# Performance work log

Measured on AMD Instinct MI355X. Metric: run time of the kernel, lower is better.

Reference implementation:

```python
import jax, jax.numpy as jnp
import numpy as np

D_MODEL = 1280
NUM_EXPERTS = 20
HEAD_DIM = D_MODEL // NUM_EXPERTS  # 64
SCALE = HEAD_DIM ** -0.5


def setup_inputs() -> dict:
    key = jax.random.key(0)
    ks = jax.random.split(key, 8)
    B, S = 4, 1024
    s_in = 1.0 / np.sqrt(D_MODEL)
    x = jax.random.normal(ks[0], (B, S, D_MODEL), dtype=jnp.float32)
    # per-expert QKV projections stacked: [E, d_model, 3*head_dim]
    wqkv = jax.random.uniform(ks[1], (NUM_EXPERTS, D_MODEL, 3 * HEAD_DIM), jnp.float32, -s_in, s_in)
    bqkv = jax.random.uniform(ks[2], (NUM_EXPERTS, 3 * HEAD_DIM), jnp.float32, -s_in, s_in)
    router_w = jax.random.uniform(ks[3], (D_MODEL, NUM_EXPERTS), jnp.float32, -s_in, s_in)
    router_b = jax.random.uniform(ks[4], (NUM_EXPERTS,), jnp.float32, -s_in, s_in)
    out_w = jax.random.uniform(ks[5], (D_MODEL, D_MODEL), jnp.float32, -s_in, s_in)
    out_b = jax.random.uniform(ks[6], (D_MODEL,), jnp.float32, -s_in, s_in)
    return {"x": x, "wqkv": wqkv, "bqkv": bqkv, "router_w": router_w,
            "router_b": router_b, "out_w": out_w, "out_b": out_b}


def reference(x, wqkv, bqkv, router_w, router_b, out_w, out_b):
    # x: [B, S, D]
    B, S, D = x.shape
    E, H = NUM_EXPERTS, HEAD_DIM
    # router softmax gates (dropout = identity in eval)
    gates = jax.nn.softmax(x @ router_w + router_b, axis=-1)  # [B, S, E]
    # per-expert QKV: [E, B, S, 3H]
    qkv = jnp.einsum('bsd,edh->ebsh', x, wqkv) + bqkv[:, None, None, :]
    q, k, v = jnp.split(qkv, 3, axis=-1)  # each [E, B, S, H]
    scores = jnp.einsum('ebqh,ebkh->ebqk', q, k) * SCALE  # [E, B, S, S]
    attn = jax.nn.softmax(scores, axis=-1)
    eo = jnp.einsum('ebqk,ebkh->ebqh', attn, v)  # [E, B, S, H]
    # gate multiply and scatter into disjoint feature slices == concat over experts
    eo = eo * jnp.transpose(gates, (2, 0, 1))[..., None]  # [E, B, S, H]
    combined = jnp.transpose(eo, (1, 2, 0, 3)).reshape(B, S, E * H)  # [B, S, D]
    return combined @ out_w + out_b
```

## Files before the change

### kernel.cpp

```cpp
#include <hip/hip_runtime.h>
#include <hip/hip_bf16.h>

#define D_MODEL 1280
#define NUM_EXPERTS 20
#define HEAD_DIM 64
#define SEQ 1024
#define BATCH 4
#define BS_TOK 4096
#define QKV_N 192
#define QKV_W 3840

typedef __attribute__((ext_vector_type(8))) short short8;
typedef __attribute__((ext_vector_type(4))) float f32x4;
typedef __attribute__((ext_vector_type(16))) float f32x16;
typedef __hip_bfloat16 bf16;

static __device__ __forceinline__ void gload_lds16(const void* g, void* l) {
  __builtin_amdgcn_global_load_lds((const __attribute__((address_space(1))) void*)g,
                                   (__attribute__((address_space(3))) void*)l, 16, 0, 0);
}

__global__ __launch_bounds__(256) void k_rwT(const float* __restrict__ in,
                                             float* __restrict__ out) {
  int i = blockIdx.x * 256 + threadIdx.x;
  if (i < D_MODEL * NUM_EXPERTS) {
    int d = i / NUM_EXPERTS, e = i % NUM_EXPERTS;
    out[e * D_MODEL + d] = in[i];
  }
}

__global__ __launch_bounds__(256) void k_gates(const float* __restrict__ x,
    const float* __restrict__ rwT, const float* __restrict__ rb,
    float* __restrict__ gates, bf16* __restrict__ xb)
{
  __shared__ float xs[4][D_MODEL];
  __shared__ float logits[4][NUM_EXPERTS];
  const int r0 = blockIdx.x * 4;
  for (int i = threadIdx.x; i < 4 * (D_MODEL / 2); i += 256) {
    int r = i / (D_MODEL / 2), d2 = (i % (D_MODEL / 2)) * 2;
    float2 v = *(const float2*)(x + (size_t)(r0 + r) * D_MODEL + d2);
    xs[r][d2] = v.x; xs[r][d2 + 1] = v.y;
    __hip_bfloat162 h;
    h.x = __float2bfloat16(v.x); h.y = __float2bfloat16(v.y);
    *(__hip_bfloat162*)(xb + (size_t)(r0 + r) * D_MODEL + d2) = h;
  }
  __syncthreads();
  const int wid = threadIdx.x >> 6, lane = threadIdx.x & 63;
  for (int e = 0; e < NUM_EXPERTS; ++e) {
    float s = 0.f;
    #pragma unroll
    for (int j = 0; j < D_MODEL / 64; ++j) {
      int d = lane + 64 * j;
      s += xs[wid][d] * rwT[e * D_MODEL + d];
    }
    #pragma unroll
    for (int m = 32; m >= 1; m >>= 1) s += __shfl_xor(s, m);
    if (lane == 0) logits[wid][e] = s + rb[e];
  }
  __syncthreads();
  if (lane < 32) {
    float v = (lane < NUM_EXPERTS) ? logits[wid][lane] : -1e30f;
    float mx = v;
    #pragma unroll
    for (int m = 16; m >= 1; m >>= 1) mx = fmaxf(mx, __shfl_xor(mx, m, 32));
    float p = (lane < NUM_EXPERTS) ? __expf(v - mx) : 0.f;
    float sum = p;
    #pragma unroll
    for (int m = 16; m >= 1; m >>= 1) sum += __shfl_xor(sum, m, 32);
    if (lane < NUM_EXPERTS)
      gates[(size_t)(r0 + wid) * NUM_EXPERTS + lane] = p / sum;
  }
}

__global__ __launch_bounds__(256) void k_transpose(const float* __restrict__ in,
    bf16* __restrict__ out, int R, int C)
{
  __shared__ float tile[32][33];
  const size_t bo = (size_t)blockIdx.z * R * C;
  const int c0 = blockIdx.x * 32, r0 = blockIdx.y * 32;
  const int tx = threadIdx.x, ty = threadIdx.y;
  #pragma unroll
  for (int i = 0; i < 4; ++i)
    tile[ty + 8*i][tx] = in[bo + (size_t)(r0 + ty + 8*i) * C + (c0 + tx)];
  __syncthreads();
  #pragma unroll
  for (int i = 0; i < 4; ++i)
    out[bo + (size_t)(c0 + ty + 8*i) * R + (r0 + tx)] =
        __float2bfloat16(tile[tx][ty + 8*i]);
}

__global__ __launch_bounds__(512, 2) void k_gemm256(
    const bf16* __restrict__ A, const bf16* __restrict__ BT,
    const float* __restrict__ bias, bf16* __restrict__ C,
    int M, int N, int K)
{
  __shared__ __align__(16) bf16 lds[4][2][256 * 32];
  const int bid = blockIdx.x;
  const int xcd = bid & 7, c = bid >> 3;
  const int m0 = (xcd * 2 + (c & 1)) * 256;
  const int n0 = (c >> 1) * 256;
  const int tid = threadIdx.x, wid = tid >> 6, lane = tid & 63;
  const int wr = wid >> 2, wcn = wid & 3;
  const int fr = lane & 15, fg = lane >> 4;
  const int nt = K / 32;

  auto STAGE = [&](int t, int buf) {
    const bf16* Ag = A + (size_t)m0 * K + t * 32;
    const bf16* Bg = BT + (size_t)n0 * K + t * 32;
    #pragma unroll
    for (int i = 0; i < 2; ++i) {
      int idx = i * 512 + tid;
      int row = idx >> 2, sc = idx & 3;
      int g = sc ^ (row & 3);
      gload_lds16(Ag + (size_t)row * K + g * 8, &lds[buf][0][idx * 8]);
    }
    #pragma unroll
    for (int i = 0; i < 2; ++i) {
      int idx = i * 512 + tid;
      int row = idx >> 2, sc = idx & 3;
      int g = sc ^ (row & 3);
      gload_lds16(Bg + (size_t)row * K + g * 8, &lds[buf][1][idx * 8]);
    }
  };

  f32x4 acc[8][4] = {};
  auto COMPUTE = [&](int buf) {
    const bf16* As_ = &lds[buf][0][0];
    const bf16* Bs_ = &lds[buf][1][0];
    short8 af[8], bfv[4];
    #pragma unroll
    for (int mi = 0; mi < 8; ++mi) {
      int row = wr * 128 + mi * 16 + fr;
      int slot = fg ^ (row & 3);
      af[mi] = *(const short8*)(As_ + row * 32 + slot * 8);
    }
    #pragma unroll
    for (int ni = 0; ni < 4; ++ni) {
      int row = wcn * 64 + ni * 16 + fr;
      int slot = fg ^ (row & 3);
      bfv[ni] = *(const short8*)(Bs_ + row * 32 + slot * 8);
    }
    __builtin_amdgcn_s_setprio(1);
    #pragma unroll
    for (int mi = 0; mi < 8; ++mi) {
      #pragma unroll
      for (int ni = 0; ni < 4; ++ni)
        acc[mi][ni] = __builtin_amdgcn_mfma_f32_16x16x32_bf16(
            af[mi], bfv[ni], acc[mi][ni], 0, 0, 0);
    }
    __builtin_amdgcn_s_setprio(0);
  };

  STAGE(0, 0); STAGE(1, 1); STAGE(2, 2);
  asm volatile("s_waitcnt vmcnt(8)" ::: "memory");
  __builtin_amdgcn_s_barrier();
  __builtin_amdgcn_sched_barrier(0);
  int buf = 0;
  for (int t = 0; t < nt - 3; ++t) {
    int nb = buf + 3; nb = (nb >= 4) ? nb - 4 : nb;
    STAGE(t + 3, nb);
    COMPUTE(buf);
    asm volatile("s_waitcnt vmcnt(8)" ::: "memory");
    __builtin_amdgcn_s_barrier();
    __builtin_amdgcn_sched_barrier(0);
    buf = (buf == 3) ? 0 : buf + 1;
  }
  COMPUTE(buf);
  asm volatile("s_waitcnt vmcnt(4)" ::: "memory");
  __builtin_amdgcn_s_barrier();
  __builtin_amdgcn_sched_barrier(0);
  buf = (buf == 3) ? 0 : buf + 1;
  COMPUTE(buf);
  asm volatile("s_waitcnt vmcnt(0)" ::: "memory");
  __builtin_amdgcn_s_barrier();
  __builtin_amdgcn_sched_barrier(0);
  buf = (buf == 3) ? 0 : buf + 1;
  COMPUTE(buf);

  #pragma unroll
  for (int mi = 0; mi < 8; ++mi) {
    const int gr = m0 + wr * 128 + mi * 16 + fg * 4;
    #pragma unroll
    for (int ni = 0; ni < 4; ++ni) {
      const int gc = n0 + wcn * 64 + ni * 16 + fr;
      const float bv = bias[gc];
      #pragma unroll
      for (int r = 0; r < 4; ++r)
        C[(size_t)(gr + r) * N + gc] = __float2bfloat16(acc[mi][ni][r] + bv);
    }
  }
}

template<bool OUT_BF16>
__global__ __launch_bounds__(256) void k_gemm(
    const bf16* __restrict__ A, const bf16* __restrict__ BT,
    const float* __restrict__ bias, void* __restrict__ C,
    int M, int N, int K)
{
  __shared__ __align__(16) bf16 As[128 * 64];
  __shared__ __align__(16) bf16 Bs[128 * 64];
  const int bid = blockIdx.x;
  const int xcd = bid & 7, c = bid >> 3;
  const int m0 = (xcd * 4 + (c & 3)) * 128;
  const int n0 = (c >> 2) * 128;
  const int tid = threadIdx.x, wid = tid >> 6, lane = tid & 63;
  const int wr = wid >> 1, wc = wid & 1;
  const int fr = lane & 15, fg = lane >> 4;
  f32x4 acc[4][4] = {};
  for (int k0 = 0; k0 < K; k0 += 64) {
    #pragma unroll
    for (int p = 0; p < 4; ++p) {
      int eidx = ((p*4 + wid)*64 + lane) * 8;
      int row = eidx >> 6, col = eidx & 63;
      gload_lds16(A + (size_t)(m0 + row)*K + k0 + col, As + eidx);
      gload_lds16(BT + (size_t)(n0 + row)*K + k0 + col, Bs + eidx);
    }
    __syncthreads();
    short8 af[2][4], bfr[2][4];
    #pragma unroll
    for (int kk = 0; kk < 2; ++kk) {
      #pragma unroll
      for (int mi = 0; mi < 4; ++mi)
        af[kk][mi] = *(const short8*)(As + (wr*64 + mi*16 + fr)*64 + kk*32 + fg*8);
      #pragma unroll
      for (int ni = 0; ni < 4; ++ni)
        bfr[kk][ni] = *(const short8*)(Bs + (wc*64 + ni*16 + fr)*64 + kk*32 + fg*8);
    }
    #pragma unroll
    for (int kk = 0; kk < 2; ++kk) {
      #pragma unroll
      for (int mi = 0; mi < 4; ++mi) {
        #pragma unroll
        for (int ni = 0; ni < 4; ++ni)
          acc[mi][ni] = __builtin_amdgcn_mfma_f32_16x16x32_bf16(
              af[kk][mi], bfr[kk][ni], acc[mi][ni], 0, 0, 0);
      }
    }
    __syncthreads();
  }
  #pragma unroll
  for (int mi = 0; mi < 4; ++mi) {
    const int gr = m0 + wr*64 + mi*16 + fg*4;
    #pragma unroll
    for (int ni = 0; ni < 4; ++ni) {
      const int gc = n0 + wc*64 + ni*16 + fr;
      const float bv = bias[gc];
      #pragma unroll
      for (int r = 0; r < 4; ++r) {
        float v = acc[mi][ni][r] + bv;
        size_t off = (size_t)(gr + r) * N + gc;
        if constexpr (OUT_BF16) ((bf16*)C)[off] = __float2bfloat16(v);
        else                    ((float*)C)[off] = v;
      }
    }
  }
}

__global__ __launch_bounds__(256) void k_attn(
    const bf16* __restrict__ qkv, const float* __restrict__ gates,
    bf16* __restrict__ combined)
{
  __shared__ __align__(16) bf16 Ks[64 * 64];
  __shared__ __align__(16) bf16 VTs[64 * 64];
  __shared__ float Ltab[128];
  const int id = blockIdx.x;
  const int xcd = id & 7, kgrp = id >> 3;
  const int qt = kgrp / 10, bel = kgrp - qt * 10;
  const int be = xcd * 10 + bel;
  const int e = be >> 2, b = be & 3;
  const int s0 = qt * 128;
  const int tid = threadIdx.x, wid = tid >> 6, lane = tid & 63;
  const int l31 = lane & 31, hi = lane >> 5;
  const bf16* base = qkv + (size_t)(b * SEQ) * QKV_W + e * QKV_N;
  const int rq = s0 + wid * 32 + l31;
  short8 qf[4];
  #pragma unroll
  for (int kc = 0; kc < 4; ++kc)
    qf[kc] = *(const short8*)(base + (size_t)rq * QKV_W + kc*16 + hi*8);
  f32x16 o0 = {}, o1 = {};
  float Mr = -1e30f, Lr = 0.f;
  const float CSC = 0.125f * 1.44269504f;
  for (int c0 = 0; c0 < SEQ; c0 += 64) {
    #pragma unroll
    for (int p = 0; p < 2; ++p) {
      int W = p*4 + wid;
      int row = W*8 + (lane >> 3);
      int g = (lane & 7) ^ W ^ (lane >> 3);
      gload_lds16(base + (size_t)(c0 + row)*QKV_W + 64 + g*8,
                  Ks + (W*64 + lane)*8);
    }
    #pragma unroll
    for (int it = 0; it < 2; ++it) {
      int key = it*32 + (tid >> 3);
      int h0b = tid & 7;
      int kc_ = key >> 3, ko = key & 7;
      union { short8 v; bf16 hh[8]; } u;
      u.v = *(const short8*)(base + (size_t)(c0 + key)*QKV_W + 128 + h0b*8);
      #pragma unroll
      for (int j = 0; j < 8; ++j) {
        int scn = kc_ ^ h0b ^ j;
        VTs[(h0b*8 + j)*64 + scn*8 + ko] = u.hh[j];
      }
    }
    __syncthreads();
    #pragma unroll
    for (int s = 0; s < 2; ++s) {
      f32x16 sc = {};
      const int krow = s*32 + l31;
      const int Sk = ((krow >> 3) ^ krow) & 7;
      #pragma unroll
      for (int kc = 0; kc < 4; ++kc) {
        int st = (kc*2 + hi) ^ Sk;
        short8 kf = *(const short8*)(Ks + krow*64 + st*8);
        sc = __builtin_amdgcn_mfma_f32_32x32x16_bf16(kf, qf[kc], sc, 0, 0, 0);
      }
      float m3 = sc[0];
      #pragma unroll
      for (int i = 1; i < 16; ++i) m3 = fmaxf(m3, sc[i]);
      float mx = fmaxf(m3, __shfl_xor(m3, 32)) * CSC;
      if (!__all(mx <= Mr + 8.0f)) {
        float Mn = fmaxf(Mr, mx);
        float so = exp2f(Mr - Mn);
        Lr *= so; Mr = Mn;
        int soi = __float_as_int(so);
        #pragma unroll
        for (int reg = 0; reg < 16; ++reg) {
          int crow = (reg & 3) + 8*(reg >> 2) + 4*hi;
          float sg = __int_as_float(__builtin_amdgcn_ds_bpermute(crow*4, soi));
          o0[reg] *= sg; o1[reg] *= sg;
        }
      }
      float p[16]; float ls = 0.f;
      #pragma unroll
      for (int i = 0; i < 16; ++i) { p[i] = exp2f(sc[i]*CSC - Mr); ls += p[i]; }
      Lr += ls + __shfl_xor(ls, 32);
      union { int w[4]; short8 v; } pf0, pf1;
      int ta, tb;
      asm("v_cvt_pk_bf16_f32 %0, %1, %2" : "=v"(ta) : "v"(p[0]), "v"(p[1]));
      asm("v_cvt_pk_bf16_f32 %0, %1, %2" : "=v"(tb) : "v"(p[4]), "v"(p[5]));
      asm volatile("v_permlane32_swap_b32 %0, %1" : "+v"(ta), "+v"(tb));
      pf0.w[0] = ta; pf0.w[2] = tb;
      asm("v_cvt_pk_bf16_f32 %0, %1, %2" : "=v"(ta) : "v"(p[2]), "v"(p[3]));
      asm("v_cvt_pk_bf16_f32 %0, %1, %2" : "=v"(tb) : "v"(p[6]), "v"(p[7]));
      asm volatile("v_permlane32_swap_b32 %0, %1" : "+v"(ta), "+v"(tb));
      pf0.w[1] = ta; pf0.w[3] = tb;
      asm("v_cvt_pk_bf16_f32 %0, %1, %2" : "=v"(ta) : "v"(p[8]), "v"(p[9]));
      asm("v_cvt_pk_bf16_f32 %0, %1, %2" : "=v"(tb) : "v"(p[12]), "v"(p[13]));
      asm volatile("v_permlane32_swap_b32 %0, %1" : "+v"(ta), "+v"(tb));
      pf1.w[0] = ta; pf1.w[2] = tb;
      asm("v_cvt_pk_bf16_f32 %0, %1, %2" : "=v"(ta) : "v"(p[10]), "v"(p[11]));
      asm("v_cvt_pk_bf16_f32 %0, %1, %2" : "=v"(tb) : "v"(p[14]), "v"(p[15]));
      asm volatile("v_permlane32_swap_b32 %0, %1" : "+v"(ta), "+v"(tb));
      pf1.w[1] = ta; pf1.w[3] = tb;
      #pragma unroll
      for (int kb = 0; kb < 2; ++kb) {
        const short8 pv = (kb == 0) ? pf0.v : pf1.v;
        #pragma unroll
        for (int hb = 0; hb < 2; ++hb) {
          int h = hb*32 + l31;
          int cc = (s*4 + kb*2 + hi) ^ (((h >> 3) ^ h) & 7);
          short8 vf = *(const short8*)(VTs + h*64 + cc*8);
          if (hb == 0) o0 = __builtin_amdgcn_mfma_f32_32x32x16_bf16(pv, vf, o0, 0, 0, 0);
          else         o1 = __builtin_amdgcn_mfma_f32_32x32x16_bf16(pv, vf, o1, 0, 0, 0);
        }
      }
    }
    __syncthreads();
  }
  if (lane < 32) {
    int q = wid*32 + lane;
    float g = gates[(size_t)(b*SEQ + s0 + q) * NUM_EXPERTS + e];
    Ltab[q] = g / Lr;
  }
  const int rowbase = b*SEQ + s0 + wid*32;
  #pragma unroll
  for (int reg = 0; reg < 16; ++reg) {
    int crow = (reg & 3) + 8*(reg >> 2) + 4*hi;
    float inv = Ltab[wid*32 + crow];
    combined[(size_t)(rowbase + crow)*D_MODEL + e*64 + l31] =
        __float2bfloat16(o0[reg] * inv);
    combined[(size_t)(rowbase + crow)*D_MODEL + e*64 + 32 + l31] =
        __float2bfloat16(o1[reg] * inv);
  }
}

extern "C" void kernel_launch(void* const* d_in, const int* in_sizes, int n_in,
                              void* d_out, int out_size, void* d_ws, size_t ws_size,
                              hipStream_t stream) {
  const float* x    = (const float*)d_in[0];
  const float* wqkv = (const float*)d_in[1];
  const float* bqkv = (const float*)d_in[2];
  const float* rw   = (const float*)d_in[3];
  const float* rb   = (const float*)d_in[4];
  const float* ow   = (const float*)d_in[5];
  const float* ob   = (const float*)d_in[6];
  char* ws = (char*)d_ws;
  bf16*  xb    = (bf16*)(ws);
  bf16*  wqkvT = (bf16*)(ws + 10485760);
  bf16*  owT   = (bf16*)(ws + 20316160);
  float* gates = (float*)(ws + 23592960);
  bf16*  qkv   = (bf16*)(ws + 23920640);
  bf16*  comb  = (bf16*)(ws + 55377920);
  float* rwT   = (float*)comb;

  k_rwT<<<(D_MODEL * NUM_EXPERTS + 255) / 256, 256, 0, stream>>>(rw, rwT);
  k_gates<<<1024, 256, 0, stream>>>(x, rwT, rb, gates, xb);
  k_transpose<<<dim3(6, 40, 20), dim3(32, 8), 0, stream>>>(wqkv, wqkvT, D_MODEL, QKV_N);
  k_transpose<<<dim3(40, 40, 1), dim3(32, 8), 0, stream>>>(ow, owT, D_MODEL, D_MODEL);
  k_gemm256<<<240, 512, 0, stream>>>(xb, wqkvT, bqkv, qkv, BS_TOK, QKV_W, D_MODEL);
  k_attn<<<640, 256, 0, stream>>>(qkv, gates, comb);
  k_gemm<false><<<8 * 4 * (D_MODEL / 128), 256, 0, stream>>>(comb, owT, ob, d_out,
                                                             BS_TOK, D_MODEL, D_MODEL);
}
```

Baseline: 181.2 us.

## Double-buffer K/V tiles in attention kernel and prefetch next tile

The attention kernel now keeps two LDS buffers for the K and transposed V tiles. It issues the global-to-LDS K load and the V register load for the next 64-key chunk before computing on the current one, which drops one barrier per iteration and hides memory latency behind the MFMA work. It also raises wave priority around the MFMA sections with s_setprio. The cost is double the LDS footprint, which may reduce occupancy, plus extra registers to hold the prefetched V data.

```diff
diff --git a/kernel.cpp b/kernel.cpp
--- a/kernel.cpp
+++ b/kernel.cpp
@@ -260,8 +260,8 @@
     const bf16* __restrict__ qkv, const float* __restrict__ gates,
     bf16* __restrict__ combined)
 {
-  __shared__ __align__(16) bf16 Ks[64 * 64];
-  __shared__ __align__(16) bf16 VTs[64 * 64];
+  __shared__ __align__(16) bf16 Ks[2][64 * 64];
+  __shared__ __align__(16) bf16 VTs[2][64 * 64];
   __shared__ float Ltab[128];
   const int id = blockIdx.x;
   const int xcd = id & 7, kgrp = id >> 3;
@@ -280,40 +280,60 @@
   f32x16 o0 = {}, o1 = {};
   float Mr = -1e30f, Lr = 0.f;
   const float CSC = 0.125f * 1.44269504f;
-  for (int c0 = 0; c0 < SEQ; c0 += 64) {
+
+  const int kst_row = (lane >> 3);
+  short8 vreg[2];
+  auto KSTAGE = [&](int c0, int bsel) {
     #pragma unroll
     for (int p = 0; p < 2; ++p) {
       int W = p*4 + wid;
-      int row = W*8 + (lane >> 3);
-      int g = (lane & 7) ^ W ^ (lane >> 3);
+      int row = W*8 + kst_row;
+      int g = (lane & 7) ^ W ^ kst_row;
       gload_lds16(base + (size_t)(c0 + row)*QKV_W + 64 + g*8,
-                  Ks + (W*64 + lane)*8);
-    }
+                  &Ks[bsel][(W*64 + lane)*8]);
+    }
+  };
+  auto VLOAD = [&](int c0) {
+    #pragma unroll
+    for (int it = 0; it < 2; ++it) {
+      int key = it*32 + (tid >> 3);
+      vreg[it] = *(const short8*)(base + (size_t)(c0 + key)*QKV_W + 128 + (tid & 7)*8);
+    }
+  };
+  auto VWRITE = [&](int bsel) {
     #pragma unroll
     for (int it = 0; it < 2; ++it) {
       int key = it*32 + (tid >> 3);
       int h0b = tid & 7;
       int kc_ = key >> 3, ko = key & 7;
-      union { short8 v; bf16 hh[8]; } u;
-      u.v = *(const short8*)(base + (size_t)(c0 + key)*QKV_W + 128 + h0b*8);
+      union { short8 v; bf16 hh[8]; } u; u.v = vreg[it];
       #pragma unroll
       for (int j = 0; j < 8; ++j) {
         int scn = kc_ ^ h0b ^ j;
-        VTs[(h0b*8 + j)*64 + scn*8 + ko] = u.hh[j];
-      }
-    }
+        VTs[bsel][(h0b*8 + j)*64 + scn*8 + ko] = u.hh[j];
+      }
+    }
+  };
+
+  KSTAGE(0, 0); VLOAD(0);
+  int bsel = 0;
+  for (int t = 0; t < SEQ / 64; ++t) {
+    VWRITE(bsel);
     __syncthreads();
+    if (t < SEQ / 64 - 1) { KSTAGE((t + 1) * 64, bsel ^ 1); VLOAD((t + 1) * 64); }
     #pragma unroll
     for (int s = 0; s < 2; ++s) {
       f32x16 sc = {};
       const int krow = s*32 + l31;
       const int Sk = ((krow >> 3) ^ krow) & 7;
+      __builtin_amdgcn_s_setprio(1);
       #pragma unroll
       for (int kc = 0; kc < 4; ++kc) {
         int st = (kc*2 + hi) ^ Sk;
-        short8 kf = *(const short8*)(Ks + krow*64 + st*8);
+        short8 kf = *(const short8*)(&Ks[bsel][krow*64 + st*8]);
         sc = __builtin_amdgcn_mfma_f32_32x32x16_bf16(kf, qf[kc], sc, 0, 0, 0);
       }
+      __builtin_amdgcn_s_setprio(0);
       float m3 = sc[0];
       #pragma unroll
       for (int i = 1; i < 16; ++i) m3 = fmaxf(m3, sc[i]);
@@ -352,6 +372,7 @@
       asm("v_cvt_pk_bf16_f32 %0, %1, %2" : "=v"(tb) : "v"(p[14]), "v"(p[15]));
       asm volatile("v_permlane32_swap_b32 %0, %1" : "+v"(ta), "+v"(tb));
       pf1.w[1] = ta; pf1.w[3] = tb;
+      __builtin_amdgcn_s_setprio(1);
       #pragma unroll
       for (int kb = 0; kb < 2; ++kb) {
         const short8 pv = (kb == 0) ? pf0.v : pf1.v;
@@ -359,19 +380,21 @@
         for (int hb = 0; hb < 2; ++hb) {
           int h = hb*32 + l31;
           int cc = (s*4 + kb*2 + hi) ^ (((h >> 3) ^ h) & 7);
-          short8 vf = *(const short8*)(VTs + h*64 + cc*8);
+          short8 vf = *(const short8*)(&VTs[bsel][h*64 + cc*8]);
           if (hb == 0) o0 = __builtin_amdgcn_mfma_f32_32x32x16_bf16(pv, vf, o0, 0, 0, 0);
           else         o1 = __builtin_amdgcn_mfma_f32_32x32x16_bf16(pv, vf, o1, 0, 0, 0);
         }
       }
-    }
-    __syncthreads();
+      __builtin_amdgcn_s_setprio(0);
+    }
+    bsel ^= 1;
   }
   if (lane < 32) {
     int q = wid*32 + lane;
     float g = gates[(size_t)(b*SEQ + s0 + q) * NUM_EXPERTS + e];
     Ltab[q] = g / Lr;
   }
+  __syncthreads();
   const int rowbase = b*SEQ + s0 + wid*32;
   #pragma unroll
   for (int reg = 0; reg < 16; ++reg) {
```

Result: no change. 181.2 us (+0.0%).
